# Performance work log

Measured on AMD Instinct MI355X. Metric: run time of the kernel, lower is better.

Reference implementation:

```python
import jax, jax.numpy as jnp
import numpy as np

K = 3        # kernel_size
GROUP = 32   # group
EPS = 1e-5   # BatchNorm eps


def setup_inputs() -> dict:
    key = jax.random.key(0)
    k1, k2 = jax.random.split(key)
    x = jax.random.normal(k1, (4, 256, 128, 128), jnp.float32)
    conv_w = jax.random.normal(k2, (GROUP * K * K, 256, K, K), jnp.float32) * 0.05
    gamma = jnp.ones((GROUP * K * K,), jnp.float32)
    beta = jnp.zeros((GROUP * K * K,), jnp.float32)
    return {"x": x, "conv_w": conv_w, "gamma": gamma, "beta": beta}


def _bilinear_align_corners(x, H, W):
    # F.upsample(..., mode='bilinear', align_corners=True)
    n, c, h, w = x.shape
    ys = jnp.linspace(0.0, h - 1.0, H)
    xs = jnp.linspace(0.0, w - 1.0, W)
    y0 = jnp.floor(ys).astype(jnp.int32)
    x0 = jnp.floor(xs).astype(jnp.int32)
    y1 = jnp.minimum(y0 + 1, h - 1)
    x1 = jnp.minimum(x0 + 1, w - 1)
    wy = (ys - y0)[None, None, :, None]
    wx = (xs - x0)[None, None, None, :]
    rows0 = x[:, :, y0, :]
    rows1 = x[:, :, y1, :]
    top = rows0[:, :, :, x0] * (1 - wx) + rows0[:, :, :, x1] * wx
    bot = rows1[:, :, :, x0] * (1 - wx) + rows1[:, :, :, x1] * wx
    return top * (1 - wy) + bot * wy


def reference(x, conv_w, gamma, beta):
    n, c, h0, w0 = x.shape
    # sigma = softmax(BN(conv(x))) over the full G*K*K channel dim
    sigma = jax.lax.conv_general_dilated(
        x, conv_w, (1, 1), 'VALID', dimension_numbers=('NCHW', 'OIHW', 'NCHW'))
    mean = sigma.mean(axis=(0, 2, 3))
    var = sigma.var(axis=(0, 2, 3))  # biased, matches BN training mode
    sigma = (sigma - mean[None, :, None, None]) * jax.lax.rsqrt(var + EPS)[None, :, None, None]
    sigma = sigma * gamma[None, :, None, None] + beta[None, :, None, None]
    sigma = jax.nn.softmax(sigma, axis=1)  # (n, G*K*K, h, w)
    h, w = sigma.shape[2], sigma.shape[3]  # h = h0-K+1, w = w0-K+1
    # Unfold: patches (n, c, K*K, h, w) with channel outer, kernel-pos inner (torch F.unfold order)
    patches = jnp.stack([x[:, :, i:i + h, j:j + w]
                         for i in range(K) for j in range(K)], axis=2)
    patches = patches.reshape(n, GROUP, c // GROUP, K * K, h, w)
    sig = sigma.reshape(n, GROUP, K * K, h, w)
    # Per-pixel, per-group weighted sum over the K*K window
    out = jnp.einsum('ngcphw,ngphw->ngchw', patches, sig).reshape(n, c, h, w)
    return _bilinear_align_corners(out, h0, w0)
```

## Files before the change

### kernel.cpp

```cpp
#include <hip/hip_runtime.h>
#include <hip/hip_bf16.h>
#include <math.h>

#define N 4
#define C 256
#define H 128
#define W 128
#define CO 288
#define OH 126
#define OW 126
#define GROUP 32
#define CPG 8
#define EPS 1e-5f

#define HW (OH*OW)
#define XSLICE (H*W)
#define XNSTRIDE (C*H*W)
#define SNSTRIDE (CO*HW)
#define LONSTRIDE (C*HW)
#define WSTRIDE (CO*256)
#define WTOT (9*CO*256)
#define XTOT (N*H*W*C)

typedef unsigned short u16;
typedef __attribute__((ext_vector_type(8))) short short8;
typedef __attribute__((ext_vector_type(4))) float float4v;

__device__ inline u16 f2bf(float v) {
    __hip_bfloat16 b = __float2bfloat16(v);
    return __builtin_bit_cast(u16, b);
}
__device__ inline float bf2f(u16 u) {
    __hip_bfloat16 b = __builtin_bit_cast(__hip_bfloat16, u);
    return __bfloat162float(b);
}

__global__ __launch_bounds__(256) void split_x_kernel(const float* __restrict__ x,
                                                      u16* __restrict__ xh,
                                                      u16* __restrict__ xl) {
    const int ci = threadIdx.x;
    const int w0 = blockIdx.x * 8;
    const int h  = blockIdx.y;
    const int n  = blockIdx.z;
    const float* src = x + ((size_t)(n*C + ci)*H + h)*W + w0;
    float4 v0 = *(const float4*)src;
    float4 v1 = *(const float4*)(src + 4);
    float vals[8] = {v0.x, v0.y, v0.z, v0.w, v1.x, v1.y, v1.z, v1.w};
    size_t obase = ((size_t)(n*H + h)*W + w0)*C + ci;
    #pragma unroll
    for (int dw = 0; dw < 8; ++dw) {
        float v = vals[dw];
        u16 hb = f2bf(v);
        xh[obase + (size_t)dw*C] = hb;
        xl[obase + (size_t)dw*C] = f2bf(v - bf2f(hb));
    }
}

__global__ __launch_bounds__(256) void split_w_kernel(const float* __restrict__ wgt,
                                                      u16* __restrict__ whT,
                                                      u16* __restrict__ wlT) {
    const int i = blockIdx.x*256 + threadIdx.x;
    const int ci = i & 255;
    const int co = (i >> 8) % CO;
    const int s  = i / (CO*256);
    float v = wgt[(size_t)co*(C*9) + (size_t)ci*9 + s];
    u16 hb = f2bf(v);
    whT[i] = hb;
    wlT[i] = f2bf(v - bf2f(hb));
}

__global__ __launch_bounds__(512, 2) void conv_mfma_kernel(const u16* __restrict__ xh,
                                                           const u16* __restrict__ whT,
                                                           float* __restrict__ sigma) {
    __shared__ __align__(16) u16 xs[25600];
    __shared__ __align__(16) u16 wsh[2*18432];

    const int tid  = threadIdx.x;
    const int wave = tid >> 6;
    const int lane = tid & 63;
    const int m16  = lane & 15;
    const int q    = lane >> 4;
    const int wr   = wave & 3;
    const int wc   = wave >> 2;
    const int ow0  = blockIdx.x * 64;
    const int oh0  = blockIdx.y * 4;
    const int n    = blockIdx.z;

    const int w_n    = (wave < 4) ? 5 : 4;
    const int w_base = (wave < 4) ? wave*320 : 1280 + (wave-4)*256;
    int wsrc[5];
    #pragma unroll
    for (int i = 0; i < 5; ++i) {
        int c = w_base + i*64 + lane;
        const int sp  = c / 1152;
        const int rem = c - sp*1152;
        const int qc  = rem / 288;
        const int co  = rem - qc*288;
        wsrc[i] = sp*WTOT + co*256 + qc*8;
    }

    int xoff[7];
    #pragma unroll
    for (int t = 0; t < 7; ++t) {
        int c = (8*t + wave)*64 + lane;
        if (c > 3167) c = 3167;
        const int spq = c / 396;
        const int rem = c - spq*396;
        const int row = rem / 66;
        const int col = rem - row*66;
        int gr = oh0 + row; if (gr > H-1) gr = H-1;
        int gc = ow0 + col; if (gc > W-1) gc = W-1;
        xoff[t] = (spq >> 2)*XTOT + ((n*H + gr)*W + gc)*C + (spq & 3)*8;
    }

    const int aoff = (q*396 + wr*66 + m16)*8;
    const int boff = (q*288 + wc*144 + m16)*8;

    float4v acc[4][9];
    #pragma unroll
    for (int mt = 0; mt < 4; ++mt)
        #pragma unroll
        for (int j = 0; j < 9; ++j) acc[mt][j] = (float4v)(0.f);

    #pragma unroll
    for (int t = 0; t < 7; ++t)
        if (t < 6 || wave < 2)
            __builtin_amdgcn_global_load_lds((const uint*)(xh + xoff[t]),
                                             (uint*)(xs + (8*t + wave)*512), 16, 0, 0);
    #pragma unroll
    for (int i = 0; i < 5; ++i)
        if (i < w_n)
            __builtin_amdgcn_global_load_lds((const uint*)(whT + wsrc[i]),
                                             (uint*)(wsh + (w_base + i*64)*8), 16, 0, 0);
    __syncthreads();

    int buf = 0;
    for (int ci0 = 0; ci0 < C; ci0 += 32) {
        #pragma unroll 1
        for (int s = 0; s < 9; ++s) {
            if (s < 8) {
                const int soff = (s+1)*WSTRIDE + ci0;
                #pragma unroll
                for (int i = 0; i < 5; ++i)
                    if (i < w_n)
                        __builtin_amdgcn_global_load_lds(
                            (const uint*)(whT + soff + wsrc[i]),
                            (uint*)(wsh + ((buf^1)*18432 + (w_base + i*64)*8)), 16, 0, 0);
            }

            const int ky = s / 3;
            const int kx = s - 3*ky;
            const int ab = aoff + (ky*66 + kx)*8;
            short8 ah0 = *(const short8*)&xs[ab];
            short8 ah1 = *(const short8*)&xs[ab + 128];
            short8 ah2 = *(const short8*)&xs[ab + 256];
            short8 ah3 = *(const short8*)&xs[ab + 384];
            short8 al0 = *(const short8*)&xs[ab + 12672];
            short8 al1 = *(const short8*)&xs[ab + 12672 + 128];
            short8 al2 = *(const short8*)&xs[ab + 12672 + 256];
            short8 al3 = *(const short8*)&xs[ab + 12672 + 384];

            if (s == 8) {
                __syncthreads();
                const int nci = ci0 + 32;
                if (nci < C) {
                    #pragma unroll
                    for (int t = 0; t < 7; ++t)
                        if (t < 6 || wave < 2)
                            __builtin_amdgcn_global_load_lds(
                                (const uint*)(xh + xoff[t] + nci),
                                (uint*)(xs + (8*t + wave)*512), 16, 0, 0);
                    #pragma unroll
                    for (int i = 0; i < 5; ++i)
                        if (i < w_n)
                            __builtin_amdgcn_global_load_lds(
                                (const uint*)(whT + nci + wsrc[i]),
                                (uint*)(wsh + ((buf^1)*18432 + (w_base + i*64)*8)), 16, 0, 0);
                }
            }

            const u16* wb = wsh + buf*18432 + boff;
            __builtin_amdgcn_s_setprio(1);
            #pragma unroll
            for (int j = 0; j < 9; ++j) {
                short8 bh = *(const short8*)&wb[j*128];
                acc[0][j] = __builtin_amdgcn_mfma_f32_16x16x32_bf16(ah0, bh, acc[0][j], 0, 0, 0);
                acc[1][j] = __builtin_amdgcn_mfma_f32_16x16x32_bf16(ah1, bh, acc[1][j], 0, 0, 0);
                acc[2][j] = __builtin_amdgcn_mfma_f32_16x16x32_bf16(ah2, bh, acc[2][j], 0, 0, 0);
                acc[3][j] = __builtin_amdgcn_mfma_f32_16x16x32_bf16(ah3, bh, acc[3][j], 0, 0, 0);
                acc[0][j] = __builtin_amdgcn_mfma_f32_16x16x32_bf16(al0, bh, acc[0][j], 0, 0, 0);
                acc[1][j] = __builtin_amdgcn_mfma_f32_16x16x32_bf16(al1, bh, acc[1][j], 0, 0, 0);
                acc[2][j] = __builtin_amdgcn_mfma_f32_16x16x32_bf16(al2, bh, acc[2][j], 0, 0, 0);
                acc[3][j] = __builtin_amdgcn_mfma_f32_16x16x32_bf16(al3, bh, acc[3][j], 0, 0, 0);
            }
            #pragma unroll
            for (int j = 0; j < 9; ++j) {
                short8 bl = *(const short8*)&wb[9216 + j*128];
                acc[0][j] = __builtin_amdgcn_mfma_f32_16x16x32_bf16(ah0, bl, acc[0][j], 0, 0, 0);
                acc[1][j] = __builtin_amdgcn_mfma_f32_16x16x32_bf16(ah1, bl, acc[1][j], 0, 0, 0);
                acc[2][j] = __builtin_amdgcn_mfma_f32_16x16x32_bf16(ah2, bl, acc[2][j], 0, 0, 0);
                acc[3][j] = __builtin_amdgcn_mfma_f32_16x16x32_bf16(ah3, bl, acc[3][j], 0, 0, 0);
            }
            __builtin_amdgcn_s_setprio(0);

            __syncthreads();
            buf ^= 1;
        }
    }

    const int oh = oh0 + wr;
    if (oh < OH) {
        #pragma unroll
        for (int mt = 0; mt < 4; ++mt) {
            const int posb = mt*16 + q*4;
            #pragma unroll
            for (int j = 0; j < 9; ++j) {
                const int co = wc*144 + j*16 + m16;
                float* dst = sigma + (size_t)n*SNSTRIDE + (size_t)co*HW + oh*OW;
                #pragma unroll
                for (int r = 0; r < 4; ++r) {
                    const int ow = ow0 + posb + r;
                    if (ow < OW) dst[ow] = acc[mt][j][r];
                }
            }
        }
    }
}

__global__ __launch_bounds__(1024) void stats_kernel(const float* __restrict__ sigma,
                                                     const float* __restrict__ gamma,
                                                     const float* __restrict__ beta,
                                                     float* __restrict__ coef) {
    const int c = blockIdx.x;
    float sum = 0.f, sq = 0.f;
    for (int n = 0; n < N; ++n) {
        const float* sp = sigma + (size_t)n*SNSTRIDE + (size_t)c*HW;
        for (int i = threadIdx.x; i < HW; i += 1024) {
            float v = sp[i];
            sum += v; sq += v * v;
        }
    }
    for (int off = 32; off > 0; off >>= 1) {
        sum += __shfl_down(sum, off, 64);
        sq  += __shfl_down(sq,  off, 64);
    }
    __shared__ float ls[16], lq[16];
    const int wid = threadIdx.x >> 6, lane = threadIdx.x & 63;
    if (lane == 0) { ls[wid] = sum; lq[wid] = sq; }
    __syncthreads();
    if (threadIdx.x == 0) {
        float S = 0.f, Q = 0.f;
        #pragma unroll
        for (int i = 0; i < 16; ++i) { S += ls[i]; Q += lq[i]; }
        const float cnt = (float)(N * HW);
        float mean = S / cnt;
        float var  = Q / cnt - mean * mean;
        float a = gamma[c] * rsqrtf(var + EPS);
        coef[c]      = a;
        coef[CO + c] = beta[c] - mean * a;
    }
}

__global__ __launch_bounds__(512) void fuse_kernel(const float* __restrict__ x,
                                                   const float* __restrict__ sigma,
                                                   const float* __restrict__ coef,
                                                   float* __restrict__ outlo,
                                                   float* __restrict__ sums) {
    __shared__ float a[CO], b[CO];
    __shared__ float xbuf[2][8*3*128];

    const int tid = threadIdx.x;
    for (int i = tid; i < CO; i += 512) {
        a[i] = coef[i];
        b[i] = coef[CO + i];
    }

    const int oh = blockIdx.x % OH;
    const int n  = blockIdx.x / OH;
    const float* xrow = x + (size_t)n * XNSTRIDE + (size_t)oh * W;

    const int f0row = tid >> 5, f0w4 = tid & 31;
    const int f1row = (512 + tid) >> 5, f1w4 = tid & 31;

    const int pos = tid >> 2;
    const int gc  = tid & 3;
    const bool act = pos < OW;
    const int hw = oh * OW + pos;
    const float* sp = sigma + (size_t)n * SNSTRIDE + hw;
    float* ob = outlo + (size_t)n * LONSTRIDE + hw;

    {
        const float* src = xrow;
        const int ch = f0row / 3, r = f0row - 3*ch;
        *(float4*)&xbuf[0][f0row*128 + f0w4*4] =
            *(const float4*)(src + (size_t)ch*XSLICE + r*W + f0w4*4);
        if (tid < 256) {
            const int ch1 = f1row / 3, r1 = f1row - 3*ch1;
            *(float4*)&xbuf[0][f1row*128 + f1w4*4] =
                *(const float4*)(src + (size_t)ch1*XSLICE + r1*W + f1w4*4);
        }
    }
    __syncthreads();

    float sum = 0.f;
    int buf = 0;
    for (int g = 0; g < GROUP; ++g) {
        if (g + 1 < GROUP) {
            const float* src = xrow + (size_t)((g+1)*CPG)*XSLICE;
            const int ch = f0row / 3, r = f0row - 3*ch;
            *(float4*)&xbuf[buf^1][f0row*128 + f0w4*4] =
                *(const float4*)(src + (size_t)ch*XSLICE + r*W + f0w4*4);
            if (tid < 256) {
                const int ch1 = f1row / 3, r1 = f1row - 3*ch1;
                *(float4*)&xbuf[buf^1][f1row*128 + f1w4*4] =
                    *(const float4*)(src + (size_t)ch1*XSLICE + r1*W + f1w4*4);
            }
        }
        if (act) {
            float acc0 = 0.f, acc1 = 0.f;
            #pragma unroll
            for (int p = 0; p < 9; ++p) {
                const int ch = g * 9 + p;
                float s = sp[(size_t)ch * HW] * a[ch] + b[ch];
                float e = __expf(s);
                sum += e;
                const int r = p / 3, cx = p - 3*r;
                const int w = pos + cx;
                acc0 += xbuf[buf][((gc*2 + 0)*3 + r)*128 + w] * e;
                acc1 += xbuf[buf][((gc*2 + 1)*3 + r)*128 + w] * e;
            }
            ob[(size_t)(g*CPG + gc*2 + 0) * HW] = acc0;
            ob[(size_t)(g*CPG + gc*2 + 1) * HW] = acc1;
        }
        __syncthreads();
        buf ^= 1;
    }
    if (act && gc == 0) sums[(size_t)n * HW + hw] = sum;
}

__global__ __launch_bounds__(256) void upsample_kernel(const float* __restrict__ lo,
                                                       const float* __restrict__ sums,
                                                       float* __restrict__ out) {
    const int idx = blockIdx.x * 256 + threadIdx.x;
    const int xi = idx & (W - 1);
    const int yi = (idx >> 7) & (H - 1);
    const int nc = idx >> 14;
    const int n  = nc >> 8;

    const float scale = 125.0f / 127.0f;
    const float sy = yi * scale;
    const float sx = xi * scale;
    int y0 = (int)sy;
    int x0 = (int)sx;
    float wy = sy - (float)y0;
    float wx = sx - (float)x0;
    int y1 = min(y0 + 1, OH - 1);
    int x1 = min(x0 + 1, OW - 1);

    const float* p  = lo + (size_t)nc * HW;
    const float* ps = sums + (size_t)n * HW;
    float v00 = p[y0 * OW + x0] / ps[y0 * OW + x0];
    float v01 = p[y0 * OW + x1] / ps[y0 * OW + x1];
    float v10 = p[y1 * OW + x0] / ps[y1 * OW + x0];
    float v11 = p[y1 * OW + x1] / ps[y1 * OW + x1];
    float top = v00 * (1.f - wx) + v01 * wx;
    float bot = v10 * (1.f - wx) + v11 * wx;
    out[idx] = top * (1.f - wy) + bot * wy;
}

extern "C" void kernel_launch(void* const* d_in, const int* in_sizes, int n_in,
                              void* d_out, int out_size, void* d_ws, size_t ws_size,
                              hipStream_t stream) {
    const float* x      = (const float*)d_in[0];
    const float* conv_w = (const float*)d_in[1];
    const float* gamma  = (const float*)d_in[2];
    const float* beta   = (const float*)d_in[3];
    float* out = (float*)d_out;
    float* ws  = (float*)d_ws;

    float* sigma = ws;
    float* coef  = ws + 18289152;
    float* outlo = ws + 18290176;
    u16* xhp = (u16*)(ws + 18290176);
    u16* xlp = xhp + (size_t)XTOT;
    u16* whT = xlp + (size_t)XTOT;
    u16* wlT = whT + (size_t)WTOT;
    float* sums = (float*)whT;

    split_x_kernel<<<dim3(16, 128, 4), 256, 0, stream>>>(x, xhp, xlp);
    split_w_kernel<<<(9*CO*256)/256, 256, 0, stream>>>(conv_w, whT, wlT);

    conv_mfma_kernel<<<dim3(2, 32, N), 512, 0, stream>>>(xhp, whT, sigma);

    stats_kernel<<<CO, 1024, 0, stream>>>(sigma, gamma, beta, coef);

    fuse_kernel<<<N * OH, 512, 0, stream>>>(x, sigma, coef, outlo, sums);

    upsample_kernel<<<(N * C * H * W) / 256, 256, 0, stream>>>(outlo, sums, out);
}
```

Measured before the change: 550.5 us.

## Split weight staging into hi/lo halves with a three-buffer LDS pipeline

The conv MFMA kernel now stages weights as separate hi and lo halves in a ring of three LDS buffers, each half-size, instead of double-buffering combined hi+lo tiles. Each kernel position is split into two phases with a prefetch two stages ahead. Explicit s_waitcnt vmcnt counts plus raw s_barrier replace __syncthreads, so outstanding loads can stay in flight across barriers. This cuts weight LDS footprint, which may allow better occupancy, and overlaps global-to-LDS traffic more deeply, at the cost of twice as many barriers and fragile hand-tuned wait counts.

```diff
diff --git a/kernel.cpp b/kernel.cpp
--- a/kernel.cpp
+++ b/kernel.cpp
@@ -73,7 +73,7 @@
                                                            const u16* __restrict__ whT,
                                                            float* __restrict__ sigma) {
     __shared__ __align__(16) u16 xs[25600];
-    __shared__ __align__(16) u16 wsh[2*18432];
+    __shared__ __align__(16) u16 wsh[3*9216];
 
     const int tid  = threadIdx.x;
     const int wave = tid >> 6;
@@ -86,17 +86,16 @@
     const int oh0  = blockIdx.y * 4;
     const int n    = blockIdx.z;
 
-    const int w_n    = (wave < 4) ? 5 : 4;
-    const int w_base = (wave < 4) ? wave*320 : 1280 + (wave-4)*256;
-    int wsrc[5];
-    #pragma unroll
-    for (int i = 0; i < 5; ++i) {
+    const int w_n    = (wave < 2) ? 3 : 2;
+    const int w_base = (wave < 2) ? wave*192 : 384 + (wave-2)*128;
+    int wsrc[3];
+    #pragma unroll
+    for (int i = 0; i < 3; ++i) {
         int c = w_base + i*64 + lane;
-        const int sp  = c / 1152;
-        const int rem = c - sp*1152;
-        const int qc  = rem / 288;
-        const int co  = rem - qc*288;
-        wsrc[i] = sp*WTOT + co*256 + qc*8;
+        if (c > 1151) c = 1151;
+        const int cq  = c / 288;
+        const int cco = c - cq*288;
+        wsrc[i] = cco*256 + cq*8;
     }
 
     int xoff[7];
@@ -128,28 +127,46 @@
             __builtin_amdgcn_global_load_lds((const uint*)(xh + xoff[t]),
                                              (uint*)(xs + (8*t + wave)*512), 16, 0, 0);
     #pragma unroll
-    for (int i = 0; i < 5; ++i)
+    for (int i = 0; i < 3; ++i)
         if (i < w_n)
             __builtin_amdgcn_global_load_lds((const uint*)(whT + wsrc[i]),
                                              (uint*)(wsh + (w_base + i*64)*8), 16, 0, 0);
-    __syncthreads();
-
-    int buf = 0;
+    #pragma unroll
+    for (int i = 0; i < 3; ++i)
+        if (i < w_n)
+            __builtin_amdgcn_global_load_lds((const uint*)(whT + WTOT + wsrc[i]),
+                                             (uint*)(wsh + 9216 + (w_base + i*64)*8), 16, 0, 0);
+    if (wave < 2) asm volatile("s_waitcnt vmcnt(3)" ::: "memory");
+    else          asm volatile("s_waitcnt vmcnt(2)" ::: "memory");
+    __builtin_amdgcn_s_barrier();
+
+    int br = 0;
     for (int ci0 = 0; ci0 < C; ci0 += 32) {
+        const int nci = ci0 + 32;
         #pragma unroll 1
         for (int s = 0; s < 9; ++s) {
-            if (s < 8) {
-                const int soff = (s+1)*WSTRIDE + ci0;
-                #pragma unroll
-                for (int i = 0; i < 5; ++i)
-                    if (i < w_n)
-                        __builtin_amdgcn_global_load_lds(
-                            (const uint*)(whT + soff + wsrc[i]),
-                            (uint*)(wsh + ((buf^1)*18432 + (w_base + i*64)*8)), 16, 0, 0);
-            }
-
             const int ky = s / 3;
             const int kx = s - 3*ky;
+
+            {
+                const int bw = (br + 2 >= 3) ? br - 1 : br + 2;
+                if (s < 8) {
+                    const int soff = (s+1)*WSTRIDE + ci0;
+                    #pragma unroll
+                    for (int i = 0; i < 3; ++i)
+                        if (i < w_n)
+                            __builtin_amdgcn_global_load_lds(
+                                (const uint*)(whT + soff + wsrc[i]),
+                                (uint*)(wsh + bw*9216 + (w_base + i*64)*8), 16, 0, 0);
+                } else if (nci < C) {
+                    #pragma unroll
+                    for (int i = 0; i < 3; ++i)
+                        if (i < w_n)
+                            __builtin_amdgcn_global_load_lds(
+                                (const uint*)(whT + nci + wsrc[i]),
+                                (uint*)(wsh + bw*9216 + (w_base + i*64)*8), 16, 0, 0);
+                }
+            }
             const int ab = aoff + (ky*66 + kx)*8;
             short8 ah0 = *(const short8*)&xs[ab];
             short8 ah1 = *(const short8*)&xs[ab + 128];
@@ -161,8 +178,8 @@
             short8 al3 = *(const short8*)&xs[ab + 12672 + 384];
 
             if (s == 8) {
-                __syncthreads();
-                const int nci = ci0 + 32;
+                asm volatile("s_waitcnt lgkmcnt(0)" ::: "memory");
+                __builtin_amdgcn_s_barrier();
                 if (nci < C) {
                     #pragma unroll
                     for (int t = 0; t < 7; ++t)
@@ -170,41 +187,82 @@
                             __builtin_amdgcn_global_load_lds(
                                 (const uint*)(xh + xoff[t] + nci),
                                 (uint*)(xs + (8*t + wave)*512), 16, 0, 0);
+                }
+            }
+
+            {
+                const u16* wb = wsh + br*9216 + boff;
+                __builtin_amdgcn_s_setprio(1);
+                #pragma unroll
+                for (int j = 0; j < 9; ++j) {
+                    short8 bh = *(const short8*)&wb[j*128];
+                    acc[0][j] = __builtin_amdgcn_mfma_f32_16x16x32_bf16(ah0, bh, acc[0][j], 0, 0, 0);
+                    acc[1][j] = __builtin_amdgcn_mfma_f32_16x16x32_bf16(ah1, bh, acc[1][j], 0, 0, 0);
+                    acc[2][j] = __builtin_amdgcn_mfma_f32_16x16x32_bf16(ah2, bh, acc[2][j], 0, 0, 0);
+                    acc[3][j] = __builtin_amdgcn_mfma_f32_16x16x32_bf16(ah3, bh, acc[3][j], 0, 0, 0);
+                    acc[0][j] = __builtin_amdgcn_mfma_f32_16x16x32_bf16(al0, bh, acc[0][j], 0, 0, 0);
+                    acc[1][j] = __builtin_amdgcn_mfma_f32_16x16x32_bf16(al1, bh, acc[1][j], 0, 0, 0);
+                    acc[2][j] = __builtin_amdgcn_mfma_f32_16x16x32_bf16(al2, bh, acc[2][j], 0, 0, 0);
+                    acc[3][j] = __builtin_amdgcn_mfma_f32_16x16x32_bf16(al3, bh, acc[3][j], 0, 0, 0);
+                }
+                __builtin_amdgcn_s_setprio(0);
+            }
+            if (s == 8) {
+                if (nci < C) {
+                    if (wave < 2) asm volatile("s_waitcnt vmcnt(10)" ::: "memory");
+                    else          asm volatile("s_waitcnt vmcnt(8)"  ::: "memory");
+                } else {
+                    asm volatile("s_waitcnt vmcnt(0)" ::: "memory");
+                }
+            } else {
+                if (wave < 2) asm volatile("s_waitcnt vmcnt(3)" ::: "memory");
+                else          asm volatile("s_waitcnt vmcnt(2)" ::: "memory");
+            }
+            asm volatile("s_waitcnt lgkmcnt(0)" ::: "memory");
+            __builtin_amdgcn_s_barrier();
+            br = (br + 1 >= 3) ? 0 : br + 1;
+
+            {
+                const int bw = (br + 2 >= 3) ? br - 1 : br + 2;
+                if (s < 8) {
+                    const int soff = WTOT + (s+1)*WSTRIDE + ci0;
                     #pragma unroll
-                    for (int i = 0; i < 5; ++i)
+                    for (int i = 0; i < 3; ++i)
                         if (i < w_n)
                             __builtin_amdgcn_global_load_lds(
-                                (const uint*)(whT + nci + wsrc[i]),
-                                (uint*)(wsh + ((buf^1)*18432 + (w_base + i*64)*8)), 16, 0, 0);
-                }
-            }
-
-            const u16* wb = wsh + buf*18432 + boff;
-            __builtin_amdgcn_s_setprio(1);
-            #pragma unroll
-            for (int j = 0; j < 9; ++j) {
-                short8 bh = *(const short8*)&wb[j*128];
-                acc[0][j] = __builtin_amdgcn_mfma_f32_16x16x32_bf16(ah0, bh, acc[0][j], 0, 0, 0);
-                acc[1][j] = __builtin_amdgcn_mfma_f32_16x16x32_bf16(ah1, bh, acc[1][j], 0, 0, 0);
-                acc[2][j] = __builtin_amdgcn_mfma_f32_16x16x32_bf16(ah2, bh, acc[2][j], 0, 0, 0);
-                acc[3][j] = __builtin_amdgcn_mfma_f32_16x16x32_bf16(ah3, bh, acc[3][j], 0, 0, 0);
-                acc[0][j] = __builtin_amdgcn_mfma_f32_16x16x32_bf16(al0, bh, acc[0][j], 0, 0, 0);
-                acc[1][j] = __builtin_amdgcn_mfma_f32_16x16x32_bf16(al1, bh, acc[1][j], 0, 0, 0);
-                acc[2][j] = __builtin_amdgcn_mfma_f32_16x16x32_bf16(al2, bh, acc[2][j], 0, 0, 0);
-                acc[3][j] = __builtin_amdgcn_mfma_f32_16x16x32_bf16(al3, bh, acc[3][j], 0, 0, 0);
-            }
-            #pragma unroll
-            for (int j = 0; j < 9; ++j) {
-                short8 bl = *(const short8*)&wb[9216 + j*128];
-                acc[0][j] = __builtin_amdgcn_mfma_f32_16x16x32_bf16(ah0, bl, acc[0][j], 0, 0, 0);
-                acc[1][j] = __builtin_amdgcn_mfma_f32_16x16x32_bf16(ah1, bl, acc[1][j], 0, 0, 0);
-                acc[2][j] = __builtin_amdgcn_mfma_f32_16x16x32_bf16(ah2, bl, acc[2][j], 0, 0, 0);
-                acc[3][j] = __builtin_amdgcn_mfma_f32_16x16x32_bf16(ah3, bl, acc[3][j], 0, 0, 0);
-            }
-            __builtin_amdgcn_s_setprio(0);
-
-            __syncthreads();
-            buf ^= 1;
+                                (const uint*)(whT + soff + wsrc[i]),
+                                (uint*)(wsh + bw*9216 + (w_base + i*64)*8), 16, 0, 0);
+                } else if (nci < C) {
+                    #pragma unroll
+                    for (int i = 0; i < 3; ++i)
+                        if (i < w_n)
+                            __builtin_amdgcn_global_load_lds(
+                                (const uint*)(whT + WTOT + nci + wsrc[i]),
+                                (uint*)(wsh + bw*9216 + (w_base + i*64)*8), 16, 0, 0);
+                }
+            }
+            {
+                const u16* wb = wsh + br*9216 + boff;
+                __builtin_amdgcn_s_setprio(1);
+                #pragma unroll
+                for (int j = 0; j < 9; ++j) {
+                    short8 bl = *(const short8*)&wb[j*128];
+                    acc[0][j] = __builtin_amdgcn_mfma_f32_16x16x32_bf16(ah0, bl, acc[0][j], 0, 0, 0);
+                    acc[1][j] = __builtin_amdgcn_mfma_f32_16x16x32_bf16(ah1, bl, acc[1][j], 0, 0, 0);
+                    acc[2][j] = __builtin_amdgcn_mfma_f32_16x16x32_bf16(ah2, bl, acc[2][j], 0, 0, 0);
+                    acc[3][j] = __builtin_amdgcn_mfma_f32_16x16x32_bf16(ah3, bl, acc[3][j], 0, 0, 0);
+                }
+                __builtin_amdgcn_s_setprio(0);
+            }
+            if (s == 8 && nci >= C) {
+                asm volatile("s_waitcnt vmcnt(0)" ::: "memory");
+            } else {
+                if (wave < 2) asm volatile("s_waitcnt vmcnt(3)" ::: "memory");
+                else          asm volatile("s_waitcnt vmcnt(2)" ::: "memory");
+            }
+            asm volatile("s_waitcnt lgkmcnt(0)" ::: "memory");
+            __builtin_amdgcn_s_barrier();
+            br = (br + 1 >= 3) ? 0 : br + 1;
         }
     }
 
```

After: 648.6 us. 17.8% more time.
